# Kernel tuning notes

Measured on AMD Instinct MI355X. Metric: run time of the kernel, lower is better.

## Reference

```python
import jax, jax.numpy as jnp
import numpy as np

N, E, G = 40000, 640000, 64
DIN, DH, H, DE = 64, 64, 2, 16
HD = H * DH  # 128
NEG_SLOPE_GAT = 0.2
NEG_SLOPE_ACT = 0.01
EPS_BN = 1e-5


def _p(k, shape, fan_in):
    return jax.random.normal(k, shape, dtype=jnp.float32) * (1.0 / np.sqrt(fan_in))


def setup_inputs() -> dict:
    key = jax.random.key(0)
    ks = jax.random.split(key, 32)
    inp = {
        'x': jax.random.normal(ks[0], (N, DIN), dtype=jnp.float32),
        'edge_index': jax.random.randint(ks[1], (2, E), 0, N, dtype=jnp.int32),
        'edge_attr': jax.random.normal(ks[2], (E, DE), dtype=jnp.float32),
        'batch': jnp.sort(jax.random.randint(ks[3], (N,), 0, G, dtype=jnp.int32)),
    }
    dims_in = [DIN, HD, HD]
    k = 4
    for i in (1, 2, 3):
        din = dims_in[i - 1]
        inp[f'w{i}l'] = _p(ks[k], (din, HD), din); k += 1
        inp[f'w{i}r'] = _p(ks[k], (din, HD), din); k += 1
        inp[f'w{i}e'] = _p(ks[k], (DE, HD), DE); k += 1
        inp[f'a{i}'] = _p(ks[k], (H, DH), DH); k += 1
        inp[f'cb{i}'] = jnp.zeros((HD,), dtype=jnp.float32)
        inp[f'g{i}'] = jnp.ones((HD,), dtype=jnp.float32)
        inp[f'bb{i}'] = jnp.zeros((HD,), dtype=jnp.float32)
    inp['fc1w'] = _p(ks[k], (HD, DH), HD); k += 1
    inp['fc1b'] = jnp.zeros((DH,), dtype=jnp.float32)
    inp['fc2w'] = _p(ks[k], (DH, 1), DH); k += 1
    inp['fc2b'] = jnp.zeros((1,), dtype=jnp.float32)
    return inp


def _gatv2(x, src, dst, ea, wl, wr, we, att, bias):
    # x:[N,din], src/dst:[Ef] (self-loops included), ea:[Ef,DE]
    xl = (x @ wl).reshape(-1, H, DH)            # source transform [N,H,C]
    xr = (x @ wr).reshape(-1, H, DH)            # target transform
    ee = (ea @ we).reshape(-1, H, DH)           # edge transform [Ef,H,C]
    m = xl[src] + xr[dst] + ee                  # GATv2 pre-activation [Ef,H,C]
    s = jnp.einsum('ehc,hc->eh', jax.nn.leaky_relu(m, NEG_SLOPE_GAT), att)
    smax = jax.ops.segment_max(s, dst, num_segments=N)
    ex = jnp.exp(s - smax[dst])
    den = jax.ops.segment_sum(ex, dst, num_segments=N)
    alpha = ex / (den[dst] + 1e-16)             # segment softmax over in-edges
    out = jax.ops.segment_sum(alpha[:, :, None] * xl[src], dst, num_segments=N)
    return out.reshape(-1, HD) + bias


def _bn(x, g, b):
    mu = jnp.mean(x, axis=0)
    var = jnp.mean((x - mu) ** 2, axis=0)
    return (x - mu) * jax.lax.rsqrt(var + EPS_BN) * g + b


def reference(x, edge_index, edge_attr, batch,
              w1l, w1r, w1e, a1, cb1, g1, bb1,
              w2l, w2r, w2e, a2, cb2, g2, bb2,
              w3l, w3r, w3e, a3, cb3, g3, bb3,
              fc1w, fc1b, fc2w, fc2b):
    src, dst = edge_index[0], edge_index[1]
    # add self-loops with fill_value='mean' edge attrs (mean over incoming edges)
    deg = jax.ops.segment_sum(jnp.ones((E,), jnp.float32), dst, num_segments=N)
    loop_attr = jax.ops.segment_sum(edge_attr, dst, num_segments=N) / jnp.clip(deg, 1.0)[:, None]
    ar = jnp.arange(N, dtype=src.dtype)
    src_f = jnp.concatenate([src, ar])
    dst_f = jnp.concatenate([dst, ar])
    ea_f = jnp.concatenate([edge_attr, loop_attr], axis=0)

    h = jax.nn.leaky_relu(_bn(_gatv2(x, src_f, dst_f, ea_f, w1l, w1r, w1e, a1, cb1), g1, bb1), NEG_SLOPE_ACT)
    h = jax.nn.leaky_relu(_bn(_gatv2(h, src_f, dst_f, ea_f, w2l, w2r, w2e, a2, cb2), g2, bb2), NEG_SLOPE_ACT)
    h = jax.nn.leaky_relu(_bn(_gatv2(h, src_f, dst_f, ea_f, w3l, w3r, w3e, a3, cb3), g3, bb3), NEG_SLOPE_ACT)

    # global mean pool over graphs
    cnt = jax.ops.segment_sum(jnp.ones((N,), jnp.float32), batch, num_segments=G)
    pooled = jax.ops.segment_sum(h, batch, num_segments=G) / jnp.clip(cnt, 1.0)[:, None]

    hh = jax.nn.relu(pooled @ fc1w + fc1b)  # dropout is identity at inference
    return hh @ fc2w + fc2b
```

## Files before the change

kernel.cpp:

```cpp
#include <hip/hip_runtime.h>
#include <math.h>

#define NN 40000
#define NE 640000
#define NG 64
#define DINV 64
#define HDV 128
#define DEV 16
#define EF (NE + NN)
#define PSPLIT 16

typedef float v2f __attribute__((ext_vector_type(2)));

__device__ __forceinline__ int chan_of_pos(int p) { return (p >> 1) + 64 * (p & 1); }

template <int CTRL>
__device__ __forceinline__ float dpp_mov_f(float x) {
    return __builtin_bit_cast(float,
        __builtin_amdgcn_update_dpp(0, __builtin_bit_cast(int, x), CTRL, 0xf, 0xf, true));
}
__device__ __forceinline__ float wave_sum64(float x) {
    x += dpp_mov_f<0x111>(x);
    x += dpp_mov_f<0x112>(x);
    x += dpp_mov_f<0x114>(x);
    x += dpp_mov_f<0x118>(x);
    x += dpp_mov_f<0x142>(x);
    x += dpp_mov_f<0x143>(x);
    return __builtin_bit_cast(float, __builtin_amdgcn_readlane(__builtin_bit_cast(int, x), 63));
}


__global__ void k_count(const int* __restrict__ dst, int* __restrict__ cnt) {
    int e = blockIdx.x * 256 + threadIdx.x;
    if (e < NE) atomicAdd(&cnt[dst[e]], 1);
}

__global__ __launch_bounds__(1024) void k_scan(const int* __restrict__ cnt, int* __restrict__ rowptr) {
    const int C = 40;
    int t = threadIdx.x;
    int start = t * C;
    int end = min(start + C, NN);
    int local = 0;
    for (int i = start; i < end; ++i) local += cnt[i] + 1;
    __shared__ int ssum[1024];
    ssum[t] = local;
    __syncthreads();
    for (int off = 1; off < 1024; off <<= 1) {
        int v = (t >= off) ? ssum[t - off] : 0;
        __syncthreads();
        ssum[t] += v;
        __syncthreads();
    }
    int running = (t == 0) ? 0 : ssum[t - 1];
    for (int i = start; i < end; ++i) {
        rowptr[i] = running;
        running += cnt[i] + 1;
    }
    if (end == NN && start < NN) rowptr[NN] = running;
}

__global__ void k_csr_init(const int* __restrict__ rowptr, int* __restrict__ cursor,
                           int* __restrict__ csr_src) {
    int n = blockIdx.x * 256 + threadIdx.x;
    if (n < NN) {
        cursor[n] = rowptr[n];
        csr_src[rowptr[n + 1] - 1] = n;
    }
}

__global__ void k_fill(const int* __restrict__ src, const int* __restrict__ dst,
                       const float* __restrict__ edge_attr,
                       int* __restrict__ cursor, int* __restrict__ csr_src, float* __restrict__ csr_ea) {
    int e = blockIdx.x * 256 + threadIdx.x;
    if (e < NE) {
        int d = dst[e];
        int p = atomicAdd(&cursor[d], 1);
        csr_src[p] = src[e];
        const float4* s4 = (const float4*)&edge_attr[(size_t)e * DEV];
        float4* d4 = (float4*)&csr_ea[(size_t)p * DEV];
        d4[0] = s4[0]; d4[1] = s4[1]; d4[2] = s4[2]; d4[3] = s4[3];
    }
}

__global__ void k_loop_attr(const int* __restrict__ rowptr, float* __restrict__ csr_ea) {
    int tid = blockIdx.x * 256 + threadIdx.x;
    int n = tid >> 4, k = tid & 15;
    if (n >= NN) return;
    int s = rowptr[n], e = rowptr[n + 1] - 1;
    float acc = 0.f;
    for (int i = s; i < e; ++i) acc += csr_ea[(size_t)i * DEV + k];
    csr_ea[(size_t)e * DEV + k] = acc / (float)max(e - s, 1);
}

__global__ void k_wperm_all(const float* __restrict__ w1l, const float* __restrict__ w1r,
                            const float* __restrict__ w2l, const float* __restrict__ w2r,
                            const float* __restrict__ w3l, const float* __restrict__ w3r,
                            float* __restrict__ wlp, float* __restrict__ wrp) {
    int i = blockIdx.x * 256 + threadIdx.x;
    if (i >= 3 * HDV * HDV) return;
    int layer = i / (HDV * HDV);
    int r = i - layer * HDV * HDV;
    int p = r & 127, kp = r >> 7;
    int K = (layer == 0) ? DINV : HDV;
    if (kp >= K) return;
    int kr = (layer == 0) ? kp : chan_of_pos(kp);
    int cc = chan_of_pos(p);
    const float* wl = (layer == 0) ? w1l : (layer == 1) ? w2l : w3l;
    const float* wr = (layer == 0) ? w1r : (layer == 1) ? w2r : w3r;
    wlp[i] = wl[kr * HDV + cc];
    wrp[i] = wr[kr * HDV + cc];
}

__global__ __launch_bounds__(256) void k_gemm(const float* __restrict__ A, int K,
                                              const float* __restrict__ Wl, const float* __restrict__ Wr,
                                              float* __restrict__ XL, float* __restrict__ XR,
                                              const double* __restrict__ bnsum, const double* __restrict__ bnsumsq,
                                              const float* __restrict__ g, const float* __restrict__ bb) {
    __shared__ float As[2][8][128];
    __shared__ float Bs[2][8][128];
    __shared__ float ssc[HDV], ssh[HDV];
    int t = threadIdx.x;
    if (bnsum && t < HDV) {
        int c = chan_of_pos(t);
        double mu = bnsum[t] * (1.0 / NN);
        double var = bnsumsq[t] * (1.0 / NN) - mu * mu;
        double inv = rsqrt(var + 1e-5);
        float sc = (float)(inv * (double)g[c]);
        ssc[t] = sc;
        ssh[t] = bb[c] - (float)mu * sc;
    }
    __syncthreads();
    int rb = blockIdx.x * 128;
    const float* __restrict__ Bg = blockIdx.y ? Wr : Wl;
    float* __restrict__ Xout = blockIdx.y ? XR : XL;
    int tx = t & 15, ty = t >> 4;
    int lr_ = t >> 1, lk = (t & 1) * 4;
    int bk = t >> 5, bc = (t & 31) * 4;

    auto loadA = [&](int k0) -> float4 {
        float4 av = (rb + lr_ < NN) ? *(const float4*)&A[(size_t)(rb + lr_) * K + k0 + lk]
                                    : float4{0.f, 0.f, 0.f, 0.f};
        if (bnsum) {
            int c0 = k0 + lk;
            av.x = fmaf(av.x, ssc[c0 + 0], ssh[c0 + 0]); av.x = fmaxf(av.x, 0.01f * av.x);
            av.y = fmaf(av.y, ssc[c0 + 1], ssh[c0 + 1]); av.y = fmaxf(av.y, 0.01f * av.y);
            av.z = fmaf(av.z, ssc[c0 + 2], ssh[c0 + 2]); av.z = fmaxf(av.z, 0.01f * av.z);
            av.w = fmaf(av.w, ssc[c0 + 3], ssh[c0 + 3]); av.w = fmaxf(av.w, 0.01f * av.w);
        }
        return av;
    };

    float4 av = loadA(0);
    float4 bv = *(const float4*)&Bg[(size_t)bk * HDV + bc];
    As[0][lk + 0][lr_] = av.x; As[0][lk + 1][lr_] = av.y; As[0][lk + 2][lr_] = av.z; As[0][lk + 3][lr_] = av.w;
    *(float4*)&Bs[0][bk][bc] = bv;
    __syncthreads();

    float acc[8][8] = {};
    int cur = 0;
    for (int k0 = 0; k0 < K; k0 += 8) {
        bool more = (k0 + 8) < K;
        if (more) {
            av = loadA(k0 + 8);
            bv = *(const float4*)&Bg[(size_t)(k0 + 8 + bk) * HDV + bc];
        }
        #pragma unroll
        for (int kk = 0; kk < 8; ++kk) {
            float a8[8], b8[8];
            *(float4*)&a8[0] = *(const float4*)&As[cur][kk][ty * 8];
            *(float4*)&a8[4] = *(const float4*)&As[cur][kk][ty * 8 + 4];
            *(float4*)&b8[0] = *(const float4*)&Bs[cur][kk][tx * 8];
            *(float4*)&b8[4] = *(const float4*)&Bs[cur][kk][tx * 8 + 4];
            #pragma unroll
            for (int ii = 0; ii < 8; ++ii)
                #pragma unroll
                for (int jj = 0; jj < 8; ++jj)
                    acc[ii][jj] = fmaf(a8[ii], b8[jj], acc[ii][jj]);
        }
        if (more) {
            int nxt = cur ^ 1;
            As[nxt][lk + 0][lr_] = av.x; As[nxt][lk + 1][lr_] = av.y;
            As[nxt][lk + 2][lr_] = av.z; As[nxt][lk + 3][lr_] = av.w;
            *(float4*)&Bs[nxt][bk][bc] = bv;
            __syncthreads();
            cur = nxt;
        }
    }
    #pragma unroll
    for (int ii = 0; ii < 8; ++ii) {
        int row = rb + ty * 8 + ii;
        if (row < NN) {
            float4 v0 = {acc[ii][0], acc[ii][1], acc[ii][2], acc[ii][3]};
            float4 v1 = {acc[ii][4], acc[ii][5], acc[ii][6], acc[ii][7]};
            *(float4*)&Xout[(size_t)row * HDV + tx * 8] = v0;
            *(float4*)&Xout[(size_t)row * HDV + tx * 8 + 4] = v1;
        }
    }
}

__device__ __forceinline__ void edge_op(const int* __restrict__ csr_src,
                                        const float* __restrict__ csr_ea, int i,
                                        const float* __restrict__ XL, int L,
                                        const v2f* __restrict__ rwe0, const v2f* __restrict__ rwe1,
                                        v2f xr, float attv0, float attv1,
                                        v2f& D, v2f& A) {
    int sx = csr_src[i];
    const v2f* eap = (const v2f*)(csr_ea + (size_t)i * DEV);
    unsigned off = ((unsigned)sx << 9) + ((unsigned)L << 3);
    v2f xl = *(const v2f*)((const char*)XL + off);
    v2f e0 = {0.f, 0.f}, e1 = {0.f, 0.f};
    #pragma unroll
    for (int j = 0; j < DEV / 2; ++j) {
        v2f ea2 = eap[j];
        e0 = __builtin_elementwise_fma(ea2, rwe0[j], e0);
        e1 = __builtin_elementwise_fma(ea2, rwe1[j], e1);
    }
    v2f m = xl + xr + v2f{e0.x + e0.y, e1.x + e1.y};
    v2f lr = __builtin_elementwise_max(m, m * 0.2f);
    float c0 = wave_sum64(lr.x * attv0);
    float c1 = wave_sum64(lr.y * attv1);
    v2f e = {__builtin_amdgcn_exp2f(c0), __builtin_amdgcn_exp2f(c1)};
    D += e;
    A = __builtin_elementwise_fma(e, xl, A);
}

__global__ __launch_bounds__(256) void k_gat(const float* __restrict__ XL, const float* __restrict__ XR,
                                             const int* __restrict__ rowptr, const int* __restrict__ csr_src,
                                             const float* __restrict__ csr_ea,
                                             const float* __restrict__ we, const float* __restrict__ att,
                                             const float* __restrict__ cb, float* __restrict__ hpre) {
    int t = threadIdx.x;
    int L = t & 63;
    int d = __builtin_amdgcn_readfirstlane(blockIdx.x * 4 + (t >> 6));
    v2f rwe0[DEV / 2], rwe1[DEV / 2];
    #pragma unroll
    for (int j = 0; j < DEV / 2; ++j) {
        rwe0[j] = v2f{we[(2 * j) * HDV + L],      we[(2 * j + 1) * HDV + L]};
        rwe1[j] = v2f{we[(2 * j) * HDV + 64 + L], we[(2 * j + 1) * HDV + 64 + L]};
    }
    const float LOG2E = 1.4426950408889634f;
    float attv0 = att[L] * LOG2E, attv1 = att[64 + L] * LOG2E;
    v2f xr = *(const v2f*)&XR[(size_t)d * HDV + 2 * L];
    int istart = rowptr[d], iend = rowptr[d + 1];
    v2f Da = {0.f, 0.f}, Db = {0.f, 0.f}, Aa = {0.f, 0.f}, Ab = {0.f, 0.f};
    int i = istart;
    if ((iend - istart) & 1) {
        edge_op(csr_src, csr_ea, i, XL, L, rwe0, rwe1, xr, attv0, attv1, Da, Aa);
        ++i;
    }
    for (; i < iend; i += 2) {
        edge_op(csr_src, csr_ea, i,     XL, L, rwe0, rwe1, xr, attv0, attv1, Da, Aa);
        edge_op(csr_src, csr_ea, i + 1, XL, L, rwe0, rwe1, xr, attv0, attv1, Db, Ab);
    }
    v2f D = Da + Db;
    v2f A = Aa + Ab;
    v2f h = A / (D + 1e-16f) + v2f{cb[L], cb[64 + L]};
    *(v2f*)&hpre[(size_t)d * HDV + 2 * L] = h;
}


__global__ __launch_bounds__(256) void k_bn_stats(const float* __restrict__ hpre,
                                                  double* __restrict__ bnsum, double* __restrict__ bnsumsq) {
    int c2 = (threadIdx.x & 63) * 2;
    int rg = threadIdx.x >> 6;
    int r0 = blockIdx.x * 250;
    v2f s = {0.f, 0.f}, q = {0.f, 0.f};
    for (int r = r0 + rg; r < r0 + 250; r += 4) {
        v2f v = *(const v2f*)&hpre[(size_t)r * HDV + c2];
        s += v;
        q = __builtin_elementwise_fma(v, v, q);
    }
    __shared__ v2f ls[256], lq[256];
    ls[threadIdx.x] = s; lq[threadIdx.x] = q;
    __syncthreads();
    if (rg == 0) {
        int b = threadIdx.x;
        s = ls[b] + ls[b + 64] + ls[b + 128] + ls[b + 192];
        q = lq[b] + lq[b + 64] + lq[b + 128] + lq[b + 192];
        atomicAdd(&bnsum[c2],     (double)s.x);
        atomicAdd(&bnsum[c2 + 1], (double)s.y);
        atomicAdd(&bnsumsq[c2],     (double)q.x);
        atomicAdd(&bnsumsq[c2 + 1], (double)q.y);
    }
}


__global__ void k_gbounds(const int* __restrict__ batch, int* __restrict__ gstart) {
    int g = threadIdx.x;
    if (g > NG) return;
    int lo = 0, hi = NN;
    while (lo < hi) {
        int mid = (lo + hi) >> 1;
        if (batch[mid] < g) lo = mid + 1; else hi = mid;
    }
    gstart[g] = lo;
}

__global__ __launch_bounds__(256) void k_pool2(const float* __restrict__ hpre, const int* __restrict__ gstart,
                                               const double* __restrict__ bnsum, const double* __restrict__ bnsumsq,
                                               const float* __restrict__ g, const float* __restrict__ bb,
                                               float* __restrict__ pooled_sum) {
    __shared__ float ssc[HDV], ssh[HDV];
    int t = threadIdx.x;
    if (t < HDV) {
        int cc = chan_of_pos(t);
        double mu = bnsum[t] * (1.0 / NN);
        double var = bnsumsq[t] * (1.0 / NN) - mu * mu;
        double inv = rsqrt(var + 1e-5);
        float sc = (float)(inv * (double)g[cc]);
        ssc[t] = sc;
        ssh[t] = bb[cc] - (float)mu * sc;
    }
    __syncthreads();
    int gr = blockIdx.x, slice = blockIdx.y;
    int s = gstart[gr], e = gstart[gr + 1];
    int c = t & 127, half = t >> 7;
    float sc = ssc[c], sh = ssh[c];
    float acc = 0.f;
    for (int r = s + slice * 2 + half; r < e; r += PSPLIT * 2) {
        float v = fmaf(hpre[(size_t)r * HDV + c], sc, sh);
        acc += fmaxf(v, 0.01f * v);
    }
    __shared__ float ls[256];
    ls[t] = acc;
    __syncthreads();
    if (half == 0) atomicAdd(&pooled_sum[gr * HDV + c], acc + ls[t + 128]);
}

__global__ __launch_bounds__(512) void k_mlp(const float* __restrict__ pooled_sum, const int* __restrict__ gstart,
                                             const float* __restrict__ fc1w, const float* __restrict__ fc1b,
                                             const float* __restrict__ fc2w, const float* __restrict__ fc2b,
                                             float* __restrict__ out) {
    __shared__ float pl[NG * HDV];
    __shared__ float hh[NG * 64];
    int t = threadIdx.x;
    for (int i = t; i < NG * HDV; i += 512) {
        int gr = i >> 7;
        float cnt = (float)max(gstart[gr + 1] - gstart[gr], 1);
        pl[i] = pooled_sum[i] / cnt;
    }
    __syncthreads();
    for (int i = t; i < NG * 64; i += 512) {
        int gr = i >> 6, c = i & 63;
        float s = fc1b[c];
        for (int p = 0; p < HDV; ++p)
            s += pl[gr * HDV + p] * fc1w[chan_of_pos(p) * 64 + c];
        hh[i] = s > 0.f ? s : 0.f;
    }
    __syncthreads();
    if (t < NG) {
        float s = fc2b[0];
        for (int k = 0; k < 64; ++k) s += hh[t * 64 + k] * fc2w[k];
        out[t] = s;
    }
}


extern "C" void kernel_launch(void* const* d_in, const int* in_sizes, int n_in,
                              void* d_out, int out_size, void* d_ws, size_t ws_size,
                              hipStream_t stream) {
    const float* x = (const float*)d_in[0];
    const int* ei = (const int*)d_in[1];
    const int* src = ei;
    const int* dst = ei + NE;
    const float* ea = (const float*)d_in[2];
    const int* batch = (const int*)d_in[3];
    const float* fc1w = (const float*)d_in[25];
    const float* fc1b = (const float*)d_in[26];
    const float* fc2w = (const float*)d_in[27];
    const float* fc2b = (const float*)d_in[28];
    float* out = (float*)d_out;

    char* ws = (char*)d_ws;
    size_t off = 0;
    auto alloc = [&](size_t bytes) -> void* {
        void* p = ws + off;
        off = (off + bytes + 255) & ~(size_t)255;
        return p;
    };

    int* cnt = (int*)alloc(NN * 4);
    double* bnsum = (double*)alloc(3 * HDV * 8);
    double* bnsumsq = (double*)alloc(3 * HDV * 8);
    float* pooled_sum = (float*)alloc(NG * HDV * 4);
    size_t zero_bytes = off;

    int* rowptr = (int*)alloc((NN + 1) * 4);
    int* cursor = (int*)alloc(NN * 4);
    int* gstart = (int*)alloc((NG + 1) * 4);
    float* wlp = (float*)alloc(3 * HDV * HDV * 4);
    float* wrp = (float*)alloc(3 * HDV * HDV * 4);
    int* csr_src = (int*)alloc(((size_t)EF + 16) * 4);
    float* csr_ea = (float*)alloc(((size_t)EF * DEV + 64) * 4);
    float* XLb = (float*)alloc((size_t)NN * HDV * 4);
    float* XRb = (float*)alloc((size_t)NN * HDV * 4);
    float* hpre = (float*)alloc((size_t)NN * HDV * 4);
    (void)ws_size; (void)in_sizes; (void)n_in; (void)out_size;

    hipMemsetAsync(d_ws, 0, zero_bytes, stream);

    k_count<<<(NE + 255) / 256, 256, 0, stream>>>(dst, cnt);
    k_scan<<<1, 1024, 0, stream>>>(cnt, rowptr);
    k_csr_init<<<(NN + 255) / 256, 256, 0, stream>>>(rowptr, cursor, csr_src);
    k_fill<<<(NE + 255) / 256, 256, 0, stream>>>(src, dst, ea, cursor, csr_src, csr_ea);
    k_loop_attr<<<(NN * DEV + 255) / 256, 256, 0, stream>>>(rowptr, csr_ea);
    k_gbounds<<<1, 128, 0, stream>>>(batch, gstart);
    k_wperm_all<<<(3 * HDV * HDV + 255) / 256, 256, 0, stream>>>(
        (const float*)d_in[4], (const float*)d_in[5],
        (const float*)d_in[11], (const float*)d_in[12],
        (const float*)d_in[18], (const float*)d_in[19], wlp, wrp);

    const float* actp = x;
    int K = DINV;
    for (int L = 0; L < 3; ++L) {
        const float* we = (const float*)d_in[4 + 7 * L + 2];
        const float* a  = (const float*)d_in[4 + 7 * L + 3];
        const float* cb = (const float*)d_in[4 + 7 * L + 4];

        const double* bs  = (L == 0) ? nullptr : bnsum + (size_t)(L - 1) * HDV;
        const double* bsq = (L == 0) ? nullptr : bnsumsq + (size_t)(L - 1) * HDV;
        const float* gg   = (L == 0) ? nullptr : (const float*)d_in[4 + 7 * (L - 1) + 5];
        const float* bbp  = (L == 0) ? nullptr : (const float*)d_in[4 + 7 * (L - 1) + 6];

        k_gemm<<<dim3((NN + 127) / 128, 2), 256, 0, stream>>>(
            actp, K, wlp + (size_t)L * HDV * HDV, wrp + (size_t)L * HDV * HDV,
            XLb, XRb, bs, bsq, gg, bbp);
        k_gat<<<NN / 4, 256, 0, stream>>>(XLb, XRb, rowptr, csr_src, csr_ea, we, a, cb, hpre);
        k_bn_stats<<<160, 256, 0, stream>>>(hpre, bnsum + (size_t)L * HDV, bnsumsq + (size_t)L * HDV);
        actp = hpre;
        K = HDV;
    }

    k_pool2<<<dim3(NG, PSPLIT), 256, 0, stream>>>(
        hpre, gstart, bnsum + 2 * HDV, bnsumsq + 2 * HDV,
        (const float*)d_in[4 + 7 * 2 + 5], (const float*)d_in[4 + 7 * 2 + 6], pooled_sum);
    k_mlp<<<1, 512, 0, stream>>>(pooled_sum, gstart, fc1w, fc1b, fc2w, fc2b, out);
}
```

Baseline: 599.2 us.

## Compute self-loop edge term in GAT kernel via linearity, drop loop_attr kernel

Removes the separate k_loop_attr kernel and the self-loop CSR slot writes. The GAT kernel instead accumulates the projected edge features of real in-edges and uses their mean as the self-loop edge term, which is valid because the edge projection is linear. The self-loop contribution is then handled after the edge loop. The edge loop is also unrolled to 4 with independent accumulators to expose more memory-level parallelism. The cost is a little extra per-edge register work, and the per-node reduction of edge attributes now runs three times, once per layer, instead of once.

Measured after the change: 616.0 us. +2.8%, slower.

```diff
diff --git a/kernel.cpp b/kernel.cpp
--- a/kernel.cpp
+++ b/kernel.cpp
@@ -59,13 +59,9 @@
     if (end == NN && start < NN) rowptr[NN] = running;
 }
 
-__global__ void k_csr_init(const int* __restrict__ rowptr, int* __restrict__ cursor,
-                           int* __restrict__ csr_src) {
+__global__ void k_csr_init(const int* __restrict__ rowptr, int* __restrict__ cursor) {
     int n = blockIdx.x * 256 + threadIdx.x;
-    if (n < NN) {
-        cursor[n] = rowptr[n];
-        csr_src[rowptr[n + 1] - 1] = n;
-    }
+    if (n < NN) cursor[n] = rowptr[n];
 }
 
 __global__ void k_fill(const int* __restrict__ src, const int* __restrict__ dst,
@@ -80,16 +76,6 @@
         float4* d4 = (float4*)&csr_ea[(size_t)p * DEV];
         d4[0] = s4[0]; d4[1] = s4[1]; d4[2] = s4[2]; d4[3] = s4[3];
     }
-}
-
-__global__ void k_loop_attr(const int* __restrict__ rowptr, float* __restrict__ csr_ea) {
-    int tid = blockIdx.x * 256 + threadIdx.x;
-    int n = tid >> 4, k = tid & 15;
-    if (n >= NN) return;
-    int s = rowptr[n], e = rowptr[n + 1] - 1;
-    float acc = 0.f;
-    for (int i = s; i < e; ++i) acc += csr_ea[(size_t)i * DEV + k];
-    csr_ea[(size_t)e * DEV + k] = acc / (float)max(e - s, 1);
 }
 
 __global__ void k_wperm_all(const float* __restrict__ w1l, const float* __restrict__ w1r,
@@ -198,32 +184,6 @@
     }
 }
 
-__device__ __forceinline__ void edge_op(const int* __restrict__ csr_src,
-                                        const float* __restrict__ csr_ea, int i,
-                                        const float* __restrict__ XL, int L,
-                                        const v2f* __restrict__ rwe0, const v2f* __restrict__ rwe1,
-                                        v2f xr, float attv0, float attv1,
-                                        v2f& D, v2f& A) {
-    int sx = csr_src[i];
-    const v2f* eap = (const v2f*)(csr_ea + (size_t)i * DEV);
-    unsigned off = ((unsigned)sx << 9) + ((unsigned)L << 3);
-    v2f xl = *(const v2f*)((const char*)XL + off);
-    v2f e0 = {0.f, 0.f}, e1 = {0.f, 0.f};
-    #pragma unroll
-    for (int j = 0; j < DEV / 2; ++j) {
-        v2f ea2 = eap[j];
-        e0 = __builtin_elementwise_fma(ea2, rwe0[j], e0);
-        e1 = __builtin_elementwise_fma(ea2, rwe1[j], e1);
-    }
-    v2f m = xl + xr + v2f{e0.x + e0.y, e1.x + e1.y};
-    v2f lr = __builtin_elementwise_max(m, m * 0.2f);
-    float c0 = wave_sum64(lr.x * attv0);
-    float c1 = wave_sum64(lr.y * attv1);
-    v2f e = {__builtin_amdgcn_exp2f(c0), __builtin_amdgcn_exp2f(c1)};
-    D += e;
-    A = __builtin_elementwise_fma(e, xl, A);
-}
-
 __global__ __launch_bounds__(256) void k_gat(const float* __restrict__ XL, const float* __restrict__ XR,
                                              const int* __restrict__ rowptr, const int* __restrict__ csr_src,
                                              const float* __restrict__ csr_ea,
@@ -241,19 +201,60 @@
     const float LOG2E = 1.4426950408889634f;
     float attv0 = att[L] * LOG2E, attv1 = att[64 + L] * LOG2E;
     v2f xr = *(const v2f*)&XR[(size_t)d * HDV + 2 * L];
-    int istart = rowptr[d], iend = rowptr[d + 1];
-    v2f Da = {0.f, 0.f}, Db = {0.f, 0.f}, Aa = {0.f, 0.f}, Ab = {0.f, 0.f};
+    int istart = rowptr[d];
+    int iend = rowptr[d + 1] - 1;
+    int deg = iend - istart;
+    v2f D0 = {0.f, 0.f}, D1 = {0.f, 0.f}, D2 = {0.f, 0.f}, D3 = {0.f, 0.f};
+    v2f A0 = {0.f, 0.f}, A1 = {0.f, 0.f}, A2 = {0.f, 0.f}, A3 = {0.f, 0.f};
+    v2f eesum = {0.f, 0.f};
+
+    auto body = [&](int i, v2f& Dk, v2f& Ak) {
+        int sx = csr_src[i];
+        const v2f* eap = (const v2f*)(csr_ea + (size_t)i * DEV);
+        unsigned off = ((unsigned)sx << 9) + ((unsigned)L << 3);
+        v2f xl = *(const v2f*)((const char*)XL + off);
+        v2f e0 = {0.f, 0.f}, e1 = {0.f, 0.f};
+        #pragma unroll
+        for (int j = 0; j < DEV / 2; ++j) {
+            v2f ea2 = eap[j];
+            e0 = __builtin_elementwise_fma(ea2, rwe0[j], e0);
+            e1 = __builtin_elementwise_fma(ea2, rwe1[j], e1);
+        }
+        v2f eev = {e0.x + e0.y, e1.x + e1.y};
+        eesum += eev;
+        v2f m = xl + xr + eev;
+        v2f lr = __builtin_elementwise_max(m, m * 0.2f);
+        float c0 = wave_sum64(lr.x * attv0);
+        float c1 = wave_sum64(lr.y * attv1);
+        v2f e = {__builtin_amdgcn_exp2f(c0), __builtin_amdgcn_exp2f(c1)};
+        Dk += e;
+        Ak = __builtin_elementwise_fma(e, xl, Ak);
+    };
+
     int i = istart;
-    if ((iend - istart) & 1) {
-        edge_op(csr_src, csr_ea, i, XL, L, rwe0, rwe1, xr, attv0, attv1, Da, Aa);
-        ++i;
-    }
-    for (; i < iend; i += 2) {
-        edge_op(csr_src, csr_ea, i,     XL, L, rwe0, rwe1, xr, attv0, attv1, Da, Aa);
-        edge_op(csr_src, csr_ea, i + 1, XL, L, rwe0, rwe1, xr, attv0, attv1, Db, Ab);
-    }
-    v2f D = Da + Db;
-    v2f A = Aa + Ab;
+    int rem = deg & 3;
+    if (rem > 0) { body(i, D0, A0); ++i; }
+    if (rem > 1) { body(i, D1, A1); ++i; }
+    if (rem > 2) { body(i, D2, A2); ++i; }
+    for (; i < iend; i += 4) {
+        body(i,     D0, A0);
+        body(i + 1, D1, A1);
+        body(i + 2, D2, A2);
+        body(i + 3, D3, A3);
+    }
+    {
+        v2f xls = *(const v2f*)&XL[(size_t)d * HDV + 2 * L];
+        v2f eeself = eesum * (1.0f / (float)max(deg, 1));
+        v2f m = xls + xr + eeself;
+        v2f lr = __builtin_elementwise_max(m, m * 0.2f);
+        float c0 = wave_sum64(lr.x * attv0);
+        float c1 = wave_sum64(lr.y * attv1);
+        v2f e = {__builtin_amdgcn_exp2f(c0), __builtin_amdgcn_exp2f(c1)};
+        D0 += e;
+        A0 = __builtin_elementwise_fma(e, xls, A0);
+    }
+    v2f D = (D0 + D1) + (D2 + D3);
+    v2f A = (A0 + A1) + (A2 + A3);
     v2f h = A / (D + 1e-16f) + v2f{cb[L], cb[64 + L]};
     *(v2f*)&hpre[(size_t)d * HDV + 2 * L] = h;
 }
@@ -401,9 +402,8 @@
 
     k_count<<<(NE + 255) / 256, 256, 0, stream>>>(dst, cnt);
     k_scan<<<1, 1024, 0, stream>>>(cnt, rowptr);
-    k_csr_init<<<(NN + 255) / 256, 256, 0, stream>>>(rowptr, cursor, csr_src);
+    k_csr_init<<<(NN + 255) / 256, 256, 0, stream>>>(rowptr, cursor);
     k_fill<<<(NE + 255) / 256, 256, 0, stream>>>(src, dst, ea, cursor, csr_src, csr_ea);
-    k_loop_attr<<<(NN * DEV + 255) / 256, 256, 0, stream>>>(rowptr, csr_ea);
     k_gbounds<<<1, 128, 0, stream>>>(batch, gstart);
     k_wperm_all<<<(3 * HDV * HDV + 255) / 256, 256, 0, stream>>>(
         (const float*)d_in[4], (const float*)d_in[5],
```
